# Kernel optimization log

Measured on AMD Instinct MI355X. Metric: run time of the kernel, lower is better.

## Reference

```python
import jax, jax.numpy as jnp
import numpy as np

WS = 7  # window_size


def _conv1x1(x, W, b):
    # 1x1 conv == channel-mixing matmul. W: [out_c, in_c], b: [out_c]
    return jnp.einsum('oc,bchw->bohw', W, x) + b[None, :, None, None]


def _window_flatten(t, ws):
    # [b, ch, H, W] -> [b, ch*nh*nw, ws*ws], matching torch unfold+contiguous+view
    b, ch, H, W = t.shape
    nh, nw = H // ws, W // ws
    t = t.reshape(b, ch, nh, ws, nw, ws).transpose(0, 1, 2, 4, 3, 5)  # [b,ch,nh,nw,ws,ws]
    return t.reshape(b, ch * nh * nw, ws * ws)


def setup_inputs() -> dict:
    key = jax.random.key(0)
    ks = jax.random.split(key, 7)
    b, c, h, w = 8, 256, 160, 160
    c8 = c // 8
    x = jax.random.normal(ks[0], (b, c, h, w), dtype=jnp.float32)
    Wq = jax.random.normal(ks[1], (c8, c), dtype=jnp.float32) * (1.0 / np.sqrt(c))
    bq = jnp.zeros((c8,), dtype=jnp.float32)
    Wk = jax.random.normal(ks[2], (c8, c), dtype=jnp.float32) * (1.0 / np.sqrt(c))
    bk = jnp.zeros((c8,), dtype=jnp.float32)
    Wv = jax.random.normal(ks[3], (c, c), dtype=jnp.float32) * (1.0 / np.sqrt(c))
    bv = jnp.zeros((c,), dtype=jnp.float32)
    return {"x": x, "Wq": Wq, "bq": bq, "Wk": Wk, "bk": bk, "Wv": Wv, "bv": bv}


def reference(x, Wq, bq, Wk, bk, Wv, bv):
    b, c, h, w = x.shape
    ws = WS
    pad_h = (ws - h % ws) % ws
    pad_w = (ws - w % ws) % ws
    xp = jnp.pad(x, ((0, 0), (0, 0), (0, pad_h), (0, pad_w)), mode='reflect')
    H, W = xp.shape[2], xp.shape[3]

    q = _window_flatten(_conv1x1(xp, Wq, bq), ws)  # [b, c8*nwin, 49]
    k = _window_flatten(_conv1x1(xp, Wk, bk), ws)  # [b, c8*nwin, 49]
    v = _window_flatten(_conv1x1(xp, Wv, bv), ws)  # [b, c*nwin, 49]

    # attn = softmax(q^T @ k) over last dim; reduction axis is channels*windows
    attn = jax.nn.softmax(jnp.einsum('bnp,bnq->bpq', q, k), axis=-1)  # [b,49,49]
    # out = v @ attn^T  -> out[b,m,i] = sum_j v[b,m,j] * attn[b,i,j]
    out = jnp.einsum('bmj,bij->bmi', v, attn)  # [b, c*nwin, 49]

    # faithful to torch .view(b, c, H, W) on contiguous [b,c,nh,nw,ws,ws] memory
    out = out.reshape(b, c, H, W)
    return out[:, :, :h, :w]
```

## Files before the change

### kernel.cpp

```cpp
#include <hip/hip_runtime.h>

#define C_ 256
#define HIN 160
#define NH 23
#define NWIN 529
#define G5 5
#define NGRP 106
#define OPLANE 25600

typedef short bf16x8 __attribute__((ext_vector_type(8)));
typedef float f32x4 __attribute__((ext_vector_type(4)));
typedef unsigned short u16x4 __attribute__((ext_vector_type(4)));

__device__ __forceinline__ unsigned short f2bf(float f) {
    union { float f; unsigned u; } v; v.f = f;
    unsigned r = v.u + 0x7FFFu + ((v.u >> 16) & 1u);
    return (unsigned short)(r >> 16);
}

__global__ void kprep(const float* __restrict__ Wq, const float* __restrict__ Wk,
                      const float* __restrict__ Wv, unsigned short* __restrict__ WvB,
                      float* __restrict__ W2t) {
    int t = blockIdx.x * 256 + threadIdx.x;
    if (t < 65536) WvB[t] = f2bf(Wv[t]);
    if (t < 16384) {
        int c = t >> 6, ch = t & 63;
        W2t[c * 64 + ch] = (ch < 32) ? Wq[ch * 256 + c] : Wk[(ch - 32) * 256 + c];
    }
}

#define QST 260
#define XST 264
__launch_bounds__(256, 2)
__global__ void k12(const float* __restrict__ x, const float* __restrict__ W2t,
                    const float* __restrict__ bq, const float* __restrict__ bk,
                    float* __restrict__ Spart) {
    __shared__ float QKs[64 * QST];
    __shared__ float Xs[8 * XST];
    __shared__ float Ws[8 * 64];

    int t = threadIdx.x;
    int g = blockIdx.x;
    int b = g & 7;
    int grp = g >> 3;
    int win0 = grp * G5;

    int wloc = t / 49, p = t % 49;
    int win = win0 + wloc;
    bool pxvalid = (t < 245) && (win < NWIN);
    const float* xp = x;
    if (pxvalid) {
        int wy = win / NH, wx = win % NH;
        int gy = wy * 7 + p / 7, gx = wx * 7 + p % 7;
        int sy = (gy < HIN) ? gy : 158;
        int sx = (gx < HIN) ? gx : 158;
        xp = x + (long)b * C_ * OPLANE + sy * HIN + sx;
    }

    int tx = t & 31, ty = t >> 5;

    float acc[8][8];
#pragma unroll
    for (int i = 0; i < 8; ++i)
#pragma unroll
        for (int j = 0; j < 8; ++j) acc[i][j] = 0.f;

    float prefX[8], prefW[2];
#pragma unroll
    for (int e = 0; e < 8; ++e) prefX[e] = pxvalid ? xp[(long)e * OPLANE] : 0.f;
#pragma unroll
    for (int i = 0; i < 2; ++i) {
        int idx = i * 256 + t, e = idx >> 6, ch = idx & 63;
        prefW[i] = W2t[e * 64 + ch];
    }

    for (int c0 = 0; c0 < 256; c0 += 8) {
#pragma unroll
        for (int e = 0; e < 8; ++e) Xs[e * XST + t] = prefX[e];
#pragma unroll
        for (int i = 0; i < 2; ++i) {
            int idx = i * 256 + t, e = idx >> 6, ch = idx & 63;
            Ws[e * 64 + ch] = prefW[i];
        }
        __syncthreads();
        if (c0 + 8 < 256) {
            int c1 = c0 + 8;
#pragma unroll
            for (int e = 0; e < 8; ++e) prefX[e] = pxvalid ? xp[(long)(c1 + e) * OPLANE] : 0.f;
#pragma unroll
            for (int i = 0; i < 2; ++i) {
                int idx = i * 256 + t, e = idx >> 6, ch = idx & 63;
                prefW[i] = W2t[(c1 + e) * 64 + ch];
            }
        }
#pragma unroll
        for (int kk = 0; kk < 8; ++kk) {
            float wv[8], xv[8];
#pragma unroll
            for (int i = 0; i < 8; ++i) wv[i] = Ws[kk * 64 + ty * 8 + i];
#pragma unroll
            for (int i = 0; i < 8; ++i) xv[i] = Xs[kk * XST + tx * 8 + i];
#pragma unroll
            for (int ci = 0; ci < 8; ++ci)
#pragma unroll
                for (int pi = 0; pi < 8; ++pi)
                    acc[ci][pi] = fmaf(wv[ci], xv[pi], acc[ci][pi]);
        }
        __syncthreads();
    }

    bool cvalid[8];
#pragma unroll
    for (int pi = 0; pi < 8; ++pi) {
        int px = tx * 8 + pi;
        int w = px / 49;
        cvalid[pi] = (px < 245) && (win0 + w < NWIN);
    }
    const float* bb = (ty < 4) ? (bq + ty * 8) : (bk + (ty - 4) * 8);
    float bias[8];
#pragma unroll
    for (int ci = 0; ci < 8; ++ci) bias[ci] = bb[ci];
#pragma unroll
    for (int ci = 0; ci < 8; ++ci) {
        int ch = ty * 8 + ci;
#pragma unroll
        for (int pi = 0; pi < 8; ++pi) {
            int px = tx * 8 + pi;
            QKs[ch * QST + px] = cvalid[pi] ? (acc[ci][pi] + bias[ci]) : 0.f;
        }
    }
    __syncthreads();

    if (t < 169) {
        int p0 = (t / 13) * 4, q0 = (t % 13) * 4;
        float s[4][4];
#pragma unroll
        for (int r = 0; r < 4; ++r)
#pragma unroll
            for (int cc = 0; cc < 4; ++cc) s[r][cc] = 0.f;
        for (int w = 0; w < G5; ++w) {
            for (int ch = 0; ch < 32; ++ch) {
                const float* qr = &QKs[ch * QST + w * 49 + p0];
                const float* kr = &QKs[(32 + ch) * QST + w * 49 + q0];
                float qv[4] = {qr[0], qr[1], qr[2], qr[3]};
                float kv[4] = {kr[0], kr[1], kr[2], kr[3]};
#pragma unroll
                for (int r = 0; r < 4; ++r)
#pragma unroll
                    for (int cc = 0; cc < 4; ++cc)
                        s[r][cc] = fmaf(qv[r], kv[cc], s[r][cc]);
            }
        }
        float* sp = Spart + (long)(b * NGRP + grp) * 2401;
#pragma unroll
        for (int r = 0; r < 4; ++r) {
            int pp = p0 + r;
            if (pp < 49) {
#pragma unroll
                for (int cc = 0; cc < 4; ++cc) {
                    int qq = q0 + cc;
                    if (qq < 49) sp[pp * 49 + qq] = s[r][cc];
                }
            }
        }
    }
}

__global__ void kred(const float* __restrict__ Spart, float* __restrict__ S) {
    int tg = blockIdx.x * 256 + threadIdx.x;
    if (tg >= 8 * 2401) return;
    int b = tg / 2401, idx = tg % 2401;
    float s = 0.f;
    for (int gr = 0; gr < NGRP; ++gr) s += Spart[(long)(b * NGRP + gr) * 2401 + idx];
    S[b * 2401 + idx] = s;
}

__global__ void ksoft(const float* __restrict__ S, unsigned short* __restrict__ attnP) {
    int b = blockIdx.x, t = threadIdx.x;
    unsigned short* row = attnP + (b * 64 + t) * 64;
    if (t < 49) {
        const float* sr = S + b * 2401 + t * 49;
        float m = -1e30f;
        for (int j = 0; j < 49; ++j) m = fmaxf(m, sr[j]);
        float den = 0.f;
        for (int j = 0; j < 49; ++j) den += expf(sr[j] - m);
        float inv = 1.f / den;
        for (int j = 0; j < 49; ++j) row[j] = f2bf(expf(sr[j] - m) * inv);
        for (int j = 49; j < 64; ++j) row[j] = 0;
    } else {
        for (int j = 0; j < 64; ++j) row[j] = 0;
    }
}

__launch_bounds__(256, 3)
__global__ void k3(const float* __restrict__ x, const unsigned short* __restrict__ WvB,
                   const unsigned short* __restrict__ attnP, const float* __restrict__ bv,
                   float* __restrict__ out) {
    __shared__ __align__(16) unsigned short Xc[256 * 40];
    __shared__ __align__(16) unsigned short Yt[64 * 264];

    int t = threadIdx.x;
    int bw = blockIdx.x;
    int b = bw & 7;
    int win = bw >> 3;
    int wy = win / NH, wx = win % NH;
    int lane = t & 63;
    int r16 = lane & 15, quad = lane >> 4, q8 = quad * 8;
    int w64 = (t >> 6) * 64;

    f32x4 zero = {0.f, 0.f, 0.f, 0.f};
    f32x4 acc1[4][4];
#pragma unroll
    for (int i = 0; i < 4; ++i)
#pragma unroll
        for (int j = 0; j < 4; ++j) acc1[i][j] = zero;

    const float* xb = x + (long)b * C_ * OPLANE;

    for (int half = 0; half < 2; ++half) {
        int jbase = half * 32;
        for (int idx = t; idx < 256 * 32; idx += 256) {
            int c = idx >> 5, j0 = idx & 31, j = jbase + j0;
            float v = 0.f;
            if (j < 49) {
                int gy = wy * 7 + j / 7, gx = wx * 7 + j % 7;
                int sy = (gy < HIN) ? gy : 158;
                int sx = (gx < HIN) ? gx : 158;
                v = xb[c * OPLANE + sy * HIN + sx];
            }
            Xc[c * 40 + j0] = f2bf(v);
        }
        __syncthreads();

        int k0 = jbase;
        bf16x8 a[4], bfr[4];
#pragma unroll
        for (int mt = 0; mt < 4; ++mt)
            a[mt] = *(const bf16x8*)&Xc[(w64 + mt * 16 + r16) * 40 + q8];
#pragma unroll
        for (int nt = 0; nt < 4; ++nt)
            bfr[nt] = *(const bf16x8*)&attnP[(b * 64 + nt * 16 + r16) * 64 + k0 + q8];
#pragma unroll
        for (int mt = 0; mt < 4; ++mt)
#pragma unroll
            for (int nt = 0; nt < 4; ++nt)
                acc1[mt][nt] = __builtin_amdgcn_mfma_f32_16x16x32_bf16(a[mt], bfr[nt], acc1[mt][nt], 0, 0, 0);
        __syncthreads();
    }

#pragma unroll
    for (int mt = 0; mt < 4; ++mt) {
        int cb = w64 + mt * 16 + quad * 4;
#pragma unroll
        for (int nt = 0; nt < 4; ++nt) {
            int ic = nt * 16 + r16;
            u16x4 pk;
            pk[0] = f2bf(acc1[mt][nt][0]);
            pk[1] = f2bf(acc1[mt][nt][1]);
            pk[2] = f2bf(acc1[mt][nt][2]);
            pk[3] = f2bf(acc1[mt][nt][3]);
            *(u16x4*)&Yt[ic * 264 + cb] = pk;
        }
    }
    __syncthreads();

    f32x4 acc2[4][4];
#pragma unroll
    for (int i = 0; i < 4; ++i)
#pragma unroll
        for (int j = 0; j < 4; ++j) acc2[i][j] = zero;

#pragma unroll
    for (int ks = 0; ks < 8; ++ks) {
        int k0 = ks * 32;
        bf16x8 a[4], bb2[4];
#pragma unroll
        for (int mt = 0; mt < 4; ++mt)
            a[mt] = *(const bf16x8*)&WvB[(w64 + mt * 16 + r16) * 256 + k0 + q8];
#pragma unroll
        for (int nt = 0; nt < 4; ++nt)
            bb2[nt] = *(const bf16x8*)&Yt[(nt * 16 + r16) * 264 + k0 + q8];
#pragma unroll
        for (int mt = 0; mt < 4; ++mt)
#pragma unroll
            for (int nt = 0; nt < 4; ++nt)
                acc2[mt][nt] = __builtin_amdgcn_mfma_f32_16x16x32_bf16(a[mt], bb2[nt], acc2[mt][nt], 0, 0, 0);
    }

    float* ob = out + (long)b * C_ * OPLANE;
#pragma unroll
    for (int nt = 0; nt < 4; ++nt) {
        int i = nt * 16 + r16;
        if (i >= 49) continue;
        int f = win * 49 + i;
        int y = f / 161, xcol = f % 161;
        if (y >= 160 || xcol >= 160) continue;
        int dst = y * 160 + xcol;
#pragma unroll
        for (int mt = 0; mt < 4; ++mt) {
            int cb = w64 + mt * 16 + quad * 4;
#pragma unroll
            for (int r = 0; r < 4; ++r) {
                int ch = cb + r;
                ob[ch * OPLANE + dst] = acc2[mt][nt][r] + bv[ch];
            }
        }
    }
}

extern "C" void kernel_launch(void* const* d_in, const int* in_sizes, int n_in,
                              void* d_out, int out_size, void* d_ws, size_t ws_size,
                              hipStream_t stream) {
    const float* x  = (const float*)d_in[0];
    const float* Wq = (const float*)d_in[1];
    const float* bq = (const float*)d_in[2];
    const float* Wk = (const float*)d_in[3];
    const float* bk = (const float*)d_in[4];
    const float* Wv = (const float*)d_in[5];
    const float* bv = (const float*)d_in[6];
    float* out = (float*)d_out;

    char* ws = (char*)d_ws;
    unsigned short* WvB   = (unsigned short*)(ws);
    float* W2t            = (float*)(ws + 131072);
    float* Spart          = (float*)(ws + 196608);
    float* S              = (float*)(ws + 196608 + 8144192);
    unsigned short* attnP = (unsigned short*)(ws + 196608 + 8144192 + 76832);

    kprep<<<dim3(256), dim3(256), 0, stream>>>(Wq, Wk, Wv, WvB, W2t);
    k12<<<dim3(8 * NGRP), dim3(256), 0, stream>>>(x, W2t, bq, bk, Spart);
    kred<<<dim3(76), dim3(256), 0, stream>>>(Spart, S);
    ksoft<<<dim3(8), dim3(64), 0, stream>>>(S, attnP);
    k3<<<dim3(8 * NWIN), dim3(256), 0, stream>>>(x, WvB, attnP, bv, out);
}
```

Baseline: 742.9 us.

## Split value projection into attention-apply then Wv GEMM via bf16 intermediate

Reorders the computation so that x is first multiplied by the attention matrix per window (kY), writing a bf16 transposed intermediate YT to workspace. A second kernel (kOut) then runs a large 256x256 Wv GEMM over pixel tiles with register-prefetched shared-memory staging and scatters the results into the output layout. This uses associativity to turn the fused per-window kernel into two well-shaped GEMMs. It costs an extra ~100MB round trip through memory and extra rounding to bf16, and it falls back to the old kernel when the workspace is too small. The reduction kernel also gets four independent accumulators.

```diff
diff --git a/kernel.cpp b/kernel.cpp
--- a/kernel.cpp
+++ b/kernel.cpp
@@ -7,10 +7,13 @@
 #define G5 5
 #define NGRP 106
 #define OPLANE 25600
+#define NP 25921
+#define NPP 25984
 
 typedef short bf16x8 __attribute__((ext_vector_type(8)));
 typedef float f32x4 __attribute__((ext_vector_type(4)));
 typedef unsigned short u16x4 __attribute__((ext_vector_type(4)));
+typedef unsigned short u16x8 __attribute__((ext_vector_type(8)));
 
 __device__ __forceinline__ unsigned short f2bf(float f) {
     union { float f; unsigned u; } v; v.f = f;
@@ -170,9 +173,17 @@
     int tg = blockIdx.x * 256 + threadIdx.x;
     if (tg >= 8 * 2401) return;
     int b = tg / 2401, idx = tg % 2401;
-    float s = 0.f;
-    for (int gr = 0; gr < NGRP; ++gr) s += Spart[(long)(b * NGRP + gr) * 2401 + idx];
-    S[b * 2401 + idx] = s;
+    const float* base = Spart + (long)b * NGRP * 2401 + idx;
+    float s0 = 0.f, s1 = 0.f, s2 = 0.f, s3 = 0.f;
+    int g = 0;
+    for (; g + 4 <= NGRP; g += 4) {
+        s0 += base[(long)(g + 0) * 2401];
+        s1 += base[(long)(g + 1) * 2401];
+        s2 += base[(long)(g + 2) * 2401];
+        s3 += base[(long)(g + 3) * 2401];
+    }
+    for (; g < NGRP; ++g) s0 += base[(long)g * 2401];
+    S[b * 2401 + idx] = (s0 + s1) + (s2 + s3);
 }
 
 __global__ void ksoft(const float* __restrict__ S, unsigned short* __restrict__ attnP) {
@@ -192,6 +203,154 @@
     }
 }
 
+__launch_bounds__(256, 4)
+__global__ void kY(const float* __restrict__ x, const unsigned short* __restrict__ attnP,
+                   unsigned short* __restrict__ YT) {
+    __shared__ __align__(16) unsigned short Xc[256 * 72];
+    int t = threadIdx.x;
+    int b = blockIdx.x & 7, win = blockIdx.x >> 3;
+    int wy = win / NH, wx = win % NH;
+    int j = t & 63, cb0 = t >> 6;
+    int jy = j / 7, jx = j % 7;
+    int gy = wy * 7 + jy, gx = wx * 7 + jx;
+    int sy = (gy < HIN) ? gy : 158;
+    int sx = (gx < HIN) ? gx : 158;
+    bool jok = (j < 49);
+    const float* xpc = x + (long)b * C_ * OPLANE + sy * HIN + sx;
+#pragma unroll 16
+    for (int c = cb0; c < 256; c += 4) {
+        float v = jok ? xpc[(long)c * OPLANE] : 0.f;
+        Xc[c * 72 + j] = f2bf(v);
+    }
+    __syncthreads();
+
+    int lane = t & 63, r16 = lane & 15, quad = lane >> 4, q8 = quad * 8;
+    int w64 = (t >> 6) * 64;
+
+    f32x4 zero = {0.f, 0.f, 0.f, 0.f};
+    f32x4 acc[4][4];
+#pragma unroll
+    for (int i = 0; i < 4; ++i)
+#pragma unroll
+        for (int jj = 0; jj < 4; ++jj) acc[i][jj] = zero;
+
+#pragma unroll
+    for (int ks = 0; ks < 2; ++ks) {
+        bf16x8 a[4], bb[4];
+#pragma unroll
+        for (int mt = 0; mt < 4; ++mt)
+            a[mt] = *(const bf16x8*)&Xc[(w64 + mt * 16 + r16) * 72 + ks * 32 + q8];
+#pragma unroll
+        for (int nt = 0; nt < 4; ++nt)
+            bb[nt] = *(const bf16x8*)&attnP[(b * 64 + nt * 16 + r16) * 64 + ks * 32 + q8];
+#pragma unroll
+        for (int mt = 0; mt < 4; ++mt)
+#pragma unroll
+            for (int nt = 0; nt < 4; ++nt)
+                acc[mt][nt] = __builtin_amdgcn_mfma_f32_16x16x32_bf16(a[mt], bb[nt], acc[mt][nt], 0, 0, 0);
+    }
+
+    unsigned short* yb = YT + (long)b * NPP * 256;
+#pragma unroll
+    for (int mt = 0; mt < 4; ++mt) {
+        int cb = w64 + mt * 16 + quad * 4;
+#pragma unroll
+        for (int nt = 0; nt < 4; ++nt) {
+            int i = nt * 16 + r16;
+            if (i < 49) {
+                int p = win * 49 + i;
+                u16x4 pk;
+                pk[0] = f2bf(acc[mt][nt][0]);
+                pk[1] = f2bf(acc[mt][nt][1]);
+                pk[2] = f2bf(acc[mt][nt][2]);
+                pk[3] = f2bf(acc[mt][nt][3]);
+                *(u16x4*)&yb[(long)p * 256 + cb] = pk;
+            }
+        }
+    }
+}
+
+__launch_bounds__(256, 3)
+__global__ void kOut(const unsigned short* __restrict__ WvB, const unsigned short* __restrict__ YT,
+                     const float* __restrict__ bv, float* __restrict__ out) {
+    __shared__ __align__(16) unsigned short Bs[128 * 72];
+    int t = threadIdx.x;
+    int b = blockIdx.x & 7;
+    int r = blockIdx.x >> 3;
+    int ct = r & 1, pt = r >> 1;
+    int ch0 = ct * 128, p0 = pt * 128;
+    const unsigned short* yb = YT + (long)b * NPP * 256;
+
+    int row = t >> 3, seg = t & 7;
+    int lane = t & 63, r16 = lane & 15, quad = lane >> 4, q8 = quad * 8;
+    int w = t >> 6;
+    int cw = (w & 1) * 64, pw = (w >> 1) * 64;
+
+    f32x4 zero = {0.f, 0.f, 0.f, 0.f};
+    f32x4 acc[4][4];
+#pragma unroll
+    for (int i = 0; i < 4; ++i)
+#pragma unroll
+        for (int jj = 0; jj < 4; ++jj) acc[i][jj] = zero;
+
+    u16x8 pf[4];
+#pragma unroll
+    for (int p4 = 0; p4 < 4; ++p4)
+        pf[p4] = *(const u16x8*)&yb[(long)(p0 + p4 * 32 + row) * 256 + seg * 8];
+
+    for (int kit = 0; kit < 4; ++kit) {
+        int c0 = kit * 64;
+#pragma unroll
+        for (int p4 = 0; p4 < 4; ++p4)
+            *(u16x8*)&Bs[(p4 * 32 + row) * 72 + seg * 8] = pf[p4];
+        __syncthreads();
+        if (kit < 3) {
+#pragma unroll
+            for (int p4 = 0; p4 < 4; ++p4)
+                pf[p4] = *(const u16x8*)&yb[(long)(p0 + p4 * 32 + row) * 256 + c0 + 64 + seg * 8];
+        }
+#pragma unroll
+        for (int ks = 0; ks < 2; ++ks) {
+            bf16x8 a[4], bb[4];
+#pragma unroll
+            for (int mt = 0; mt < 4; ++mt)
+                a[mt] = *(const bf16x8*)&WvB[(ch0 + cw + mt * 16 + r16) * 256 + c0 + ks * 32 + q8];
+#pragma unroll
+            for (int nt = 0; nt < 4; ++nt)
+                bb[nt] = *(const bf16x8*)&Bs[(pw + nt * 16 + r16) * 72 + ks * 32 + q8];
+#pragma unroll
+            for (int mt = 0; mt < 4; ++mt)
+#pragma unroll
+                for (int nt = 0; nt < 4; ++nt)
+                    acc[mt][nt] = __builtin_amdgcn_mfma_f32_16x16x32_bf16(a[mt], bb[nt], acc[mt][nt], 0, 0, 0);
+        }
+        __syncthreads();
+    }
+
+    float bvv[4][4];
+#pragma unroll
+    for (int mt = 0; mt < 4; ++mt)
+#pragma unroll
+        for (int rr = 0; rr < 4; ++rr) bvv[mt][rr] = bv[ch0 + cw + mt * 16 + quad * 4 + rr];
+
+    float* ob = out + (long)b * C_ * OPLANE;
+#pragma unroll
+    for (int nt = 0; nt < 4; ++nt) {
+        int p = p0 + pw + nt * 16 + r16;
+        if (p >= NP) continue;
+        int y = p / 161, xx = p % 161;
+        if (y >= 160 || xx >= 160) continue;
+        int dst = y * 160 + xx;
+#pragma unroll
+        for (int mt = 0; mt < 4; ++mt) {
+            int cb = ch0 + cw + mt * 16 + quad * 4;
+#pragma unroll
+            for (int rr = 0; rr < 4; ++rr)
+                ob[(long)(cb + rr) * OPLANE + dst] = acc[mt][nt][rr] + bvv[mt][rr];
+        }
+    }
+}
+
 __launch_bounds__(256, 3)
 __global__ void k3(const float* __restrict__ x, const unsigned short* __restrict__ WvB,
                    const unsigned short* __restrict__ attnP, const float* __restrict__ bv,
@@ -324,12 +483,20 @@
     unsigned short* WvB   = (unsigned short*)(ws);
     float* W2t            = (float*)(ws + 131072);
     float* Spart          = (float*)(ws + 196608);
-    float* S              = (float*)(ws + 196608 + 8144192);
-    unsigned short* attnP = (unsigned short*)(ws + 196608 + 8144192 + 76832);
+    float* S              = (float*)(ws + 8340800);
+    unsigned short* attnP = (unsigned short*)(ws + 8417632);
+    unsigned short* YT    = (unsigned short*)(ws + 8483328);
+
+    size_t need = 8483328ull + 106430464ull;
 
     kprep<<<dim3(256), dim3(256), 0, stream>>>(Wq, Wk, Wv, WvB, W2t);
     k12<<<dim3(8 * NGRP), dim3(256), 0, stream>>>(x, W2t, bq, bk, Spart);
     kred<<<dim3(76), dim3(256), 0, stream>>>(Spart, S);
     ksoft<<<dim3(8), dim3(64), 0, stream>>>(S, attnP);
-    k3<<<dim3(8 * NWIN), dim3(256), 0, stream>>>(x, WvB, attnP, bv, out);
-}
+    if (ws_size >= need) {
+        kY<<<dim3(8 * NWIN), dim3(256), 0, stream>>>(x, attnP, YT);
+        kOut<<<dim3(8 * 203 * 2), dim3(256), 0, stream>>>(WvB, YT, bv, out);
+    } else {
+        k3<<<dim3(8 * NWIN), dim3(256), 0, stream>>>(x, WvB, attnP, bv, out);
+    }
+}
```

New measurement: 745.5 us. Within noise of the previous version (+0.3%).
